# Kernel tuning notes

Measured on AMD Instinct MI355X. Metric: run time of the kernel, lower is better.

The kernel has to match this reference:

```python
import jax, jax.numpy as jnp
import numpy as np

I = 4  # input size
H = 4  # hidden size


def setup_inputs() -> dict:
    key = jax.random.key(0)
    ks = jax.random.split(key, 7)
    T, B = 2048, 8192
    s = 1.0 / np.sqrt(H)  # torch LSTM/Linear init scale
    x = jax.random.normal(ks[0], (T, B, I), dtype=jnp.float32)
    w_ih = jax.random.uniform(ks[1], (4 * H, I), minval=-s, maxval=s, dtype=jnp.float32)
    w_hh = jax.random.uniform(ks[2], (4 * H, H), minval=-s, maxval=s, dtype=jnp.float32)
    b_ih = jax.random.uniform(ks[3], (4 * H,), minval=-s, maxval=s, dtype=jnp.float32)
    b_hh = jax.random.uniform(ks[4], (4 * H,), minval=-s, maxval=s, dtype=jnp.float32)
    w_lin = jax.random.uniform(ks[5], (1, H), minval=-0.5, maxval=0.5, dtype=jnp.float32)
    b_lin = jax.random.uniform(ks[6], (1,), minval=-0.5, maxval=0.5, dtype=jnp.float32)
    return {"x": x, "w_ih": w_ih, "w_hh": w_hh, "b_ih": b_ih, "b_hh": b_hh,
            "w_lin": w_lin, "b_lin": b_lin}


def _lstm_scan(x, w_ih, w_hh, b_ih, b_hh):
    # x: (T, B, I). PyTorch gate order: i, f, g, o.
    T, B, _ = x.shape
    b = b_ih + b_hh  # (4H,)
    # Precompute input projections for all timesteps: (T, B, 4H)
    xg = jnp.einsum('tbi,gi->tbg', x, w_ih) + b

    def step(carry, xg_t):
        h, c = carry  # (B, H) each
        gates = xg_t + h @ w_hh.T  # (B, 4H)
        i, f, g, o = jnp.split(gates, 4, axis=-1)
        i = jax.nn.sigmoid(i)
        f = jax.nn.sigmoid(f)
        g = jnp.tanh(g)
        o = jax.nn.sigmoid(o)
        c = f * c + i * g
        h = o * jnp.tanh(c)
        return (h, c), h

    h0 = jnp.zeros((B, H), dtype=x.dtype)
    c0 = jnp.zeros((B, H), dtype=x.dtype)
    _, hs = jax.lax.scan(step, (h0, c0), xg)
    return hs  # (T, B, H)


def reference(x, w_ih, w_hh, b_ih, b_hh, w_lin, b_lin):
    hs = _lstm_scan(x, w_ih, w_hh, b_ih, b_hh)           # (T, B, H)
    out = jnp.einsum('tbh,oh->tbo', hs, w_lin) + b_lin   # (T, B, 1)
    return jax.nn.sigmoid(out)
```

## Files before the change

### kernel.cpp

```cpp
#include <hip/hip_runtime.h>

#define T_DIM 2048
#define B_DIM 8192
#define PH    256
#define SPH   8

using f32x2 = __attribute__((ext_vector_type(2))) float;

__device__ __forceinline__ float dpp_qxor1(float v) {
  int i = __float_as_int(v);
  return __int_as_float(__builtin_amdgcn_update_dpp(i, i, 0xB1, 0xF, 0xF, false));
}
__device__ __forceinline__ float dpp_qxor2(float v) {
  int i = __float_as_int(v);
  return __int_as_float(__builtin_amdgcn_update_dpp(i, i, 0x4E, 0xF, 0xF, false));
}
__device__ __forceinline__ float dpp_qxor3(float v) {
  int i = __float_as_int(v);
  return __int_as_float(__builtin_amdgcn_update_dpp(i, i, 0x1B, 0xF, 0xF, false));
}
__device__ __forceinline__ float dpp_hmirror(float v) {
  int i = __float_as_int(v);
  return __int_as_float(__builtin_amdgcn_update_dpp(i, i, 0x141, 0xF, 0xF, false));
}

__global__ __launch_bounds__(768) void lstm_sr_kernel(
    const float* __restrict__ x,
    const float* __restrict__ w_ih, const float* __restrict__ w_hh,
    const float* __restrict__ b_ih, const float* __restrict__ b_hh,
    const float* __restrict__ w_lin, const float* __restrict__ b_lin,
    float* __restrict__ out)
{
  __shared__ f32x2 xaBuf[2][4][SPH][64];
  __shared__ float hnBuf[2][4][64][9];

  const int tid  = threadIdx.x;
  const int wid  = tid >> 6;
  const int lane = tid & 63;
  const int pair = wid & 3;

  const float L2E = 1.4426950408889634f;
  const float cm2 = -2.0f * L2E;

  const int l = lane & 7;
  const int half1 = (l >> 2) & 1;
  const int e = (l & 3) ^ (half1 ? 3 : 0);
  const int grp = lane >> 3;
  const int rA = half1 * 4 + e;
  const int rB = 8 + half1 * 4 + e;
  const float sclA = -L2E;
  const float sclB = half1 ? -L2E : -2.0f * L2E;

  if (wid < 4) {
    __builtin_amdgcn_s_setprio(1);
    float whhA[4], whhB[4];
    #pragma unroll
    for (int k = 0; k < 4; ++k) {
      const int j = e ^ k;
      whhA[k] = sclA * w_hh[rA * 4 + j];
      whhB[k] = sclB * w_hh[rB * 4 + j];
    }
    const float sB = half1 ? 1.0f : 2.0f * cm2;
    const float oB = half1 ? 0.0f : -cm2;
    float ct = 0.0f, h0 = 0.0f, h1v = 0.0f, h2v = 0.0f, h3v = 0.0f;

    __syncthreads();

    for (int p = 0; p < PH; ++p) {
      const int d = p & 1;
      f32x2 xa2[SPH];
      #pragma unroll
      for (int k = 0; k < SPH; ++k) xa2[k] = xaBuf[d][pair][k][lane];

      #pragma unroll
      for (int k = 0; k < SPH; ++k) {
        float uA = fmaf(whhA[1], h1v, fmaf(whhA[0], h0, xa2[k][0]));
        const float vA = fmaf(whhA[3], h3v, whhA[2] * h2v);
        uA += vA;
        float uB = fmaf(whhB[1], h1v, fmaf(whhB[0], h0, xa2[k][1]));
        const float vB = fmaf(whhB[3], h3v, whhB[2] * h2v);
        uB += vB;

        const float EA = __builtin_amdgcn_exp2f(uA);
        const float EB = __builtin_amdgcn_exp2f(uB);
        const float dA = 1.0f + EA;
        const float dB = 1.0f + EB;
        const float r  = __builtin_amdgcn_rcpf(dA * dB);
        const float aA = r * dB;
        const float yB = r * dA;
        const float aB = fmaf(sB, yB, oB);

        const float Z = half1 ? aA : aA * aB;
        const float W = dpp_hmirror(Z);
        const float F = half1 ? Z : W;
        const float P = half1 ? W : Z;
        ct = fmaf(F, ct, P);

        const float zc = __builtin_amdgcn_exp2f(ct);
        const float rc = __builtin_amdgcn_rcpf(1.0f + zc);
        const float Ox = dpp_hmirror(aB);
        const float ov = half1 ? aB : Ox;
        const float tc = fmaf(2.0f, rc, -1.0f);
        const float hn = ov * tc;
        h0  = hn;
        h1v = dpp_qxor1(hn);
        h2v = dpp_qxor2(hn);
        h3v = dpp_qxor3(hn);
        hnBuf[d][pair][lane][k] = hn;
      }
      __syncthreads();
    }
  } else if (wid < 8) {
    const int b = blockIdx.x * 32 + pair * 8 + grp;
    float wihA[4], wihB[4];
    #pragma unroll
    for (int k = 0; k < 4; ++k) {
      const int j = e ^ k;
      wihA[k] = sclA * w_ih[rA * 4 + j];
      wihB[k] = sclB * w_ih[rB * 4 + j];
    }
    const float biasA = sclA * (b_ih[rA] + b_hh[rA]);
    const float biasB = sclB * (b_ih[rB] + b_hh[rB]);

    const int XS = B_DIM * 4;
    const int xoff = b * 4 + e;

    float xc[SPH], xn[SPH];

    auto load8 = [&](float (&dst)[SPH], int ph) {
      const int base = xoff + ((ph & (PH - 1)) * SPH) * XS;
      #pragma unroll
      for (int k = 0; k < SPH; ++k) dst[k] = x[base + k * XS];
    };
    auto projWrite = [&](const float (&xr)[SPH], int dd) {
      #pragma unroll
      for (int k = 0; k < SPH; ++k) {
        const float xe = xr[k];
        const float x1 = dpp_qxor1(xe);
        const float x2 = dpp_qxor2(xe);
        const float x3 = dpp_qxor3(xe);
        f32x2 acc;
        float a = fmaf(wihA[0], xe, biasA);
        a = fmaf(wihA[1], x1, a);
        a = fmaf(wihA[2], x2, a);
        a = fmaf(wihA[3], x3, a);
        float bb = fmaf(wihB[0], xe, biasB);
        bb = fmaf(wihB[1], x1, bb);
        bb = fmaf(wihB[2], x2, bb);
        bb = fmaf(wihB[3], x3, bb);
        acc[0] = a;
        acc[1] = bb;
        xaBuf[dd][pair][k][lane] = acc;
      }
    };

    load8(xc, 0);
    projWrite(xc, 0);
    load8(xn, 1);
    __syncthreads();

    for (int pp = 0; pp < PH; pp += 2) {
      projWrite(xn, 1);
      load8(xc, pp + 2);
      __syncthreads();
      projWrite(xc, 0);
      load8(xn, pp + 3);
      __syncthreads();
    }
  } else {
    const int og = lane & 7, oj = lane >> 3;
    const int ob = blockIdx.x * 32 + pair * 8 + og;
    float wl[4];
    #pragma unroll
    for (int j = 0; j < 4; ++j) wl[j] = -L2E * w_lin[j];
    const float blin = -L2E * b_lin[0];

    __syncthreads();

    for (int p = 0; p < PH; ++p) {
      __syncthreads();
      const int dh = p & 1;
      const float v0 = hnBuf[dh][pair][og * 8 + 0][oj];
      const float v1 = hnBuf[dh][pair][og * 8 + 1][oj];
      const float v2 = hnBuf[dh][pair][og * 8 + 2][oj];
      const float v3 = hnBuf[dh][pair][og * 8 + 3][oj];
      float m = fmaf(wl[0], v0, blin);
      m = fmaf(wl[1], v1, m);
      m = fmaf(wl[2], v2, m);
      m = fmaf(wl[3], v3, m);
      const float o = __builtin_amdgcn_rcpf(1.0f + __builtin_amdgcn_exp2f(m));
      out[(size_t)(p * SPH + oj) * B_DIM + ob] = o;
    }
  }
}

extern "C" void kernel_launch(void* const* d_in, const int* in_sizes, int n_in,
                              void* d_out, int out_size, void* d_ws, size_t ws_size,
                              hipStream_t stream) {
  const float* x     = (const float*)d_in[0];
  const float* w_ih  = (const float*)d_in[1];
  const float* w_hh  = (const float*)d_in[2];
  const float* b_ih  = (const float*)d_in[3];
  const float* b_hh  = (const float*)d_in[4];
  const float* w_lin = (const float*)d_in[5];
  const float* b_lin = (const float*)d_in[6];
  float* out = (float*)d_out;

  dim3 block(768);
  dim3 grid(B_DIM / 32);
  hipLaunchKernelGGL(lstm_sr_kernel, grid, block, 0, stream,
                     x, w_ih, w_hh, b_ih, b_hh, w_lin, b_lin, out);
}
```

Baseline: 238.6 us.

## Compute all four gates per lane, halving recurrence lanes per batch element

Each recurrence lane now handles one hidden unit and evaluates all four gates itself (4 lanes per batch element instead of 8). This removes the cross-half DPP mirror exchanges and the lane-divergent selects. The block shrinks to 384 threads with 2 recurrence, 2 projection and 2 output waves, and the projection writes float4 gate vectors. In exchange each recurrence lane does twice the serial exp/rcp work per step, which lengthens the dependent chain per timestep, while fewer waves are needed per batch element.

```diff
diff --git a/kernel.cpp b/kernel.cpp
--- a/kernel.cpp
+++ b/kernel.cpp
@@ -5,8 +5,6 @@
 #define PH    256
 #define SPH   8
 
-using f32x2 = __attribute__((ext_vector_type(2))) float;
-
 __device__ __forceinline__ float dpp_qxor1(float v) {
   int i = __float_as_int(v);
   return __int_as_float(__builtin_amdgcn_update_dpp(i, i, 0xB1, 0xF, 0xF, false));
@@ -19,111 +17,105 @@
   int i = __float_as_int(v);
   return __int_as_float(__builtin_amdgcn_update_dpp(i, i, 0x1B, 0xF, 0xF, false));
 }
-__device__ __forceinline__ float dpp_hmirror(float v) {
-  int i = __float_as_int(v);
-  return __int_as_float(__builtin_amdgcn_update_dpp(i, i, 0x141, 0xF, 0xF, false));
-}
-
-__global__ __launch_bounds__(768) void lstm_sr_kernel(
+
+__global__ __launch_bounds__(384) void lstm_l4_kernel(
     const float* __restrict__ x,
     const float* __restrict__ w_ih, const float* __restrict__ w_hh,
     const float* __restrict__ b_ih, const float* __restrict__ b_hh,
     const float* __restrict__ w_lin, const float* __restrict__ b_lin,
     float* __restrict__ out)
 {
-  __shared__ f32x2 xaBuf[2][4][SPH][64];
-  __shared__ float hnBuf[2][4][64][9];
+  __shared__ float4 xaBuf[2][2][SPH][64];
+  __shared__ float  hnBuf[2][2][64][9];
 
   const int tid  = threadIdx.x;
   const int wid  = tid >> 6;
   const int lane = tid & 63;
-  const int pair = wid & 3;
+  const int rw   = wid & 1;
 
   const float L2E = 1.4426950408889634f;
   const float cm2 = -2.0f * L2E;
 
-  const int l = lane & 7;
-  const int half1 = (l >> 2) & 1;
-  const int e = (l & 3) ^ (half1 ? 3 : 0);
-  const int grp = lane >> 3;
-  const int rA = half1 * 4 + e;
-  const int rB = 8 + half1 * 4 + e;
-  const float sclA = -L2E;
-  const float sclB = half1 ? -L2E : -2.0f * L2E;
-
-  if (wid < 4) {
+  const int g = lane >> 2;
+  const int j = lane & 3;
+
+  if (wid < 2) {
     __builtin_amdgcn_s_setprio(1);
-    float whhA[4], whhB[4];
+    float wi[4], wf[4], wg[4], wo[4];
     #pragma unroll
-    for (int k = 0; k < 4; ++k) {
-      const int j = e ^ k;
-      whhA[k] = sclA * w_hh[rA * 4 + j];
-      whhB[k] = sclB * w_hh[rB * 4 + j];
-    }
-    const float sB = half1 ? 1.0f : 2.0f * cm2;
-    const float oB = half1 ? 0.0f : -cm2;
+    for (int m = 0; m < 4; ++m) {
+      const int jm = j ^ m;
+      wi[m] = -L2E * w_hh[(0  + j) * 4 + jm];
+      wf[m] = -L2E * w_hh[(4  + j) * 4 + jm];
+      wg[m] = cm2  * w_hh[(8  + j) * 4 + jm];
+      wo[m] = -L2E * w_hh[(12 + j) * 4 + jm];
+    }
     float ct = 0.0f, h0 = 0.0f, h1v = 0.0f, h2v = 0.0f, h3v = 0.0f;
 
     __syncthreads();
 
     for (int p = 0; p < PH; ++p) {
       const int d = p & 1;
-      f32x2 xa2[SPH];
-      #pragma unroll
-      for (int k = 0; k < SPH; ++k) xa2[k] = xaBuf[d][pair][k][lane];
+      float4 xa[SPH];
+      #pragma unroll
+      for (int k = 0; k < SPH; ++k) xa[k] = xaBuf[d][rw][k][lane];
 
       #pragma unroll
       for (int k = 0; k < SPH; ++k) {
-        float uA = fmaf(whhA[1], h1v, fmaf(whhA[0], h0, xa2[k][0]));
-        const float vA = fmaf(whhA[3], h3v, whhA[2] * h2v);
-        uA += vA;
-        float uB = fmaf(whhB[1], h1v, fmaf(whhB[0], h0, xa2[k][1]));
-        const float vB = fmaf(whhB[3], h3v, whhB[2] * h2v);
-        uB += vB;
-
-        const float EA = __builtin_amdgcn_exp2f(uA);
-        const float EB = __builtin_amdgcn_exp2f(uB);
-        const float dA = 1.0f + EA;
-        const float dB = 1.0f + EB;
-        const float r  = __builtin_amdgcn_rcpf(dA * dB);
-        const float aA = r * dB;
-        const float yB = r * dA;
-        const float aB = fmaf(sB, yB, oB);
-
-        const float Z = half1 ? aA : aA * aB;
-        const float W = dpp_hmirror(Z);
-        const float F = half1 ? Z : W;
-        const float P = half1 ? W : Z;
-        ct = fmaf(F, ct, P);
-
+        float ti = fmaf(wi[1], h1v, fmaf(wi[0], h0, xa[k].x));
+        ti += fmaf(wi[3], h3v, wi[2] * h2v);
+        float tf = fmaf(wf[1], h1v, fmaf(wf[0], h0, xa[k].y));
+        tf += fmaf(wf[3], h3v, wf[2] * h2v);
+        float tg = fmaf(wg[1], h1v, fmaf(wg[0], h0, xa[k].z));
+        tg += fmaf(wg[3], h3v, wg[2] * h2v);
+        float to = fmaf(wo[1], h1v, fmaf(wo[0], h0, xa[k].w));
+        to += fmaf(wo[3], h3v, wo[2] * h2v);
+
+        const float Ei = __builtin_amdgcn_exp2f(ti);
+        const float Ef = __builtin_amdgcn_exp2f(tf);
+        const float Eg = __builtin_amdgcn_exp2f(tg);
+        const float Eo = __builtin_amdgcn_exp2f(to);
+        const float di  = 1.0f + Ei, df_ = 1.0f + Ef;
+        const float dg  = 1.0f + Eg, do_ = 1.0f + Eo;
+        const float r1 = __builtin_amdgcn_rcpf(di * df_);
+        const float r2 = __builtin_amdgcn_rcpf(dg * do_);
+        const float gi = r1 * df_;
+        const float gf = r1 * di;
+        const float yG = r2 * do_;
+        const float go = r2 * dg;
+        const float tgp = fmaf(2.0f * cm2, yG, -cm2);
+        const float P = gi * tgp;
+        ct = fmaf(gf, ct, P);
         const float zc = __builtin_amdgcn_exp2f(ct);
         const float rc = __builtin_amdgcn_rcpf(1.0f + zc);
-        const float Ox = dpp_hmirror(aB);
-        const float ov = half1 ? aB : Ox;
-        const float tc = fmaf(2.0f, rc, -1.0f);
-        const float hn = ov * tc;
+        const float o2 = go + go;
+        const float hn = fmaf(o2, rc, -go);
         h0  = hn;
         h1v = dpp_qxor1(hn);
         h2v = dpp_qxor2(hn);
         h3v = dpp_qxor3(hn);
-        hnBuf[d][pair][lane][k] = hn;
+        hnBuf[d][rw][lane][k] = hn;
       }
       __syncthreads();
     }
-  } else if (wid < 8) {
-    const int b = blockIdx.x * 32 + pair * 8 + grp;
-    float wihA[4], wihB[4];
+  } else if (wid < 4) {
+    const int b = blockIdx.x * 32 + rw * 16 + g;
+    float wii[4], wif[4], wig[4], wio[4];
     #pragma unroll
-    for (int k = 0; k < 4; ++k) {
-      const int j = e ^ k;
-      wihA[k] = sclA * w_ih[rA * 4 + j];
-      wihB[k] = sclB * w_ih[rB * 4 + j];
-    }
-    const float biasA = sclA * (b_ih[rA] + b_hh[rA]);
-    const float biasB = sclB * (b_ih[rB] + b_hh[rB]);
+    for (int m = 0; m < 4; ++m) {
+      const int jm = j ^ m;
+      wii[m] = -L2E * w_ih[(0  + j) * 4 + jm];
+      wif[m] = -L2E * w_ih[(4  + j) * 4 + jm];
+      wig[m] = cm2  * w_ih[(8  + j) * 4 + jm];
+      wio[m] = -L2E * w_ih[(12 + j) * 4 + jm];
+    }
+    const float bi = -L2E * (b_ih[j]      + b_hh[j]);
+    const float bf = -L2E * (b_ih[4 + j]  + b_hh[4 + j]);
+    const float bg = cm2  * (b_ih[8 + j]  + b_hh[8 + j]);
+    const float bo = -L2E * (b_ih[12 + j] + b_hh[12 + j]);
 
     const int XS = B_DIM * 4;
-    const int xoff = b * 4 + e;
+    const int xoff = b * 4 + j;
 
     float xc[SPH], xn[SPH];
 
@@ -139,18 +131,15 @@
         const float x1 = dpp_qxor1(xe);
         const float x2 = dpp_qxor2(xe);
         const float x3 = dpp_qxor3(xe);
-        f32x2 acc;
-        float a = fmaf(wihA[0], xe, biasA);
-        a = fmaf(wihA[1], x1, a);
-        a = fmaf(wihA[2], x2, a);
-        a = fmaf(wihA[3], x3, a);
-        float bb = fmaf(wihB[0], xe, biasB);
-        bb = fmaf(wihB[1], x1, bb);
-        bb = fmaf(wihB[2], x2, bb);
-        bb = fmaf(wihB[3], x3, bb);
-        acc[0] = a;
-        acc[1] = bb;
-        xaBuf[dd][pair][k][lane] = acc;
+        float ui = fmaf(wii[0], xe, bi);
+        ui = fmaf(wii[1], x1, ui); ui = fmaf(wii[2], x2, ui); ui = fmaf(wii[3], x3, ui);
+        float uf = fmaf(wif[0], xe, bf);
+        uf = fmaf(wif[1], x1, uf); uf = fmaf(wif[2], x2, uf); uf = fmaf(wif[3], x3, uf);
+        float ug = fmaf(wig[0], xe, bg);
+        ug = fmaf(wig[1], x1, ug); ug = fmaf(wig[2], x2, ug); ug = fmaf(wig[3], x3, ug);
+        float uo = fmaf(wio[0], xe, bo);
+        uo = fmaf(wio[1], x1, uo); uo = fmaf(wio[2], x2, uo); uo = fmaf(wio[3], x3, uo);
+        xaBuf[dd][rw][k][lane] = make_float4(ui, uf, ug, uo);
       }
     };
 
@@ -168,11 +157,12 @@
       __syncthreads();
     }
   } else {
-    const int og = lane & 7, oj = lane >> 3;
-    const int ob = blockIdx.x * 32 + pair * 8 + og;
+    const int ge = lane & 15;
+    const int su = lane >> 4;
+    const int ob = blockIdx.x * 32 + rw * 16 + ge;
     float wl[4];
     #pragma unroll
-    for (int j = 0; j < 4; ++j) wl[j] = -L2E * w_lin[j];
+    for (int m = 0; m < 4; ++m) wl[m] = -L2E * w_lin[m];
     const float blin = -L2E * b_lin[0];
 
     __syncthreads();
@@ -180,16 +170,20 @@
     for (int p = 0; p < PH; ++p) {
       __syncthreads();
       const int dh = p & 1;
-      const float v0 = hnBuf[dh][pair][og * 8 + 0][oj];
-      const float v1 = hnBuf[dh][pair][og * 8 + 1][oj];
-      const float v2 = hnBuf[dh][pair][og * 8 + 2][oj];
-      const float v3 = hnBuf[dh][pair][og * 8 + 3][oj];
-      float m = fmaf(wl[0], v0, blin);
-      m = fmaf(wl[1], v1, m);
-      m = fmaf(wl[2], v2, m);
-      m = fmaf(wl[3], v3, m);
-      const float o = __builtin_amdgcn_rcpf(1.0f + __builtin_amdgcn_exp2f(m));
-      out[(size_t)(p * SPH + oj) * B_DIM + ob] = o;
+      #pragma unroll
+      for (int s2 = 0; s2 < 2; ++s2) {
+        const int s = su + s2 * 4;
+        const float v0 = hnBuf[dh][rw][4 * ge + 0][s];
+        const float v1 = hnBuf[dh][rw][4 * ge + 1][s];
+        const float v2 = hnBuf[dh][rw][4 * ge + 2][s];
+        const float v3 = hnBuf[dh][rw][4 * ge + 3][s];
+        float mm = fmaf(wl[0], v0, blin);
+        mm = fmaf(wl[1], v1, mm);
+        mm = fmaf(wl[2], v2, mm);
+        mm = fmaf(wl[3], v3, mm);
+        const float o = __builtin_amdgcn_rcpf(1.0f + __builtin_amdgcn_exp2f(mm));
+        out[(size_t)(p * SPH + s) * B_DIM + ob] = o;
+      }
     }
   }
 }
@@ -206,8 +200,8 @@
   const float* b_lin = (const float*)d_in[6];
   float* out = (float*)d_out;
 
-  dim3 block(768);
+  dim3 block(384);
   dim3 grid(B_DIM / 32);
-  hipLaunchKernelGGL(lstm_sr_kernel, grid, block, 0, stream,
+  hipLaunchKernelGGL(lstm_l4_kernel, grid, block, 0, stream,
                      x, w_ih, w_hh, b_ih, b_hh, w_lin, b_lin, out);
 }
```

Measured after the change: 236.6 us. No clear change (-0.8%).
